# Optimization experiments

Measured on AMD Instinct MI355X. Metric: run time of the kernel, lower is better.

Reference implementation:

```python
import jax, jax.numpy as jnp
import numpy as np

K = 2            # top-k experts
TEMPERATURE = 1.0
EPS = 1e-9


def setup_inputs() -> dict:
    key = jax.random.key(0)
    k1, k2 = jax.random.split(key)
    B, S, D = 4, 4096, 4096
    G, E = 4, 64
    x = jax.random.normal(k1, (B, S, D), dtype=jnp.float32)
    # stacked gate weights, one [E, D] Linear weight per gate head
    W = jax.random.normal(k2, (G, E, D), dtype=jnp.float32) * 0.02
    return {"x": x, "W": W}


def reference(x, W):
    # per-head logits over experts: [B, S, G, E]; jitter disabled (eval / jitter_noise=0)
    logits = jnp.einsum('bsd,ged->bsge', x, W) * (1.0 / TEMPERATURE)
    probs = jax.nn.softmax(logits, axis=-1)          # softmax per head
    probs_full = probs.mean(axis=2)                  # consensus over heads: [B, S, E]
    topk_vals, idx = jax.lax.top_k(probs_full, K)    # sorted descending, matches aten.topk
    den = jnp.sum(topk_vals, axis=-1, keepdims=True)
    scores = topk_vals / jnp.maximum(den, EPS)       # clamp_min(den, 1e-9)
    pf = jax.lax.stop_gradient(probs_full)           # aux stats under no_grad
    importance = pf.mean(axis=(0, 1))                # [E]
    load = (pf > 0.0).astype(pf.dtype).mean(axis=(0, 1))  # [E]
    return idx, scores, probs_full, importance, load
```

## Files before the change

kernel.cpp:

```cpp
#include <hip/hip_runtime.h>

typedef _Float16 f16x8 __attribute__((ext_vector_type(8)));
typedef float    f32x4 __attribute__((ext_vector_type(4)));

#define MROWS 16384
#define NCOLS 256
#define KDIM  4096
#define BM    64
#define BK    32

#define OUT_SCORES 32768
#define OUT_PF     65536
#define OUT_IMP    1114112
#define OUT_LOAD   1114176

__global__ __launch_bounds__(256) void wprep(const float* __restrict__ W,
                                             _Float16* __restrict__ wfHi,
                                             _Float16* __restrict__ wfLo) {
    int t   = blockIdx.x * 256 + threadIdx.x;
    int l   = t & 63;
    int NT  = (t >> 6) & 15;
    int ksg = t >> 10;
    int n   = NT * 16 + (l & 15);
    int k   = ksg * 32 + ((l >> 4) << 3);
    const float* src = W + ((size_t)n * KDIM + (size_t)k);
    f16x8 hi, lo;
#pragma unroll
    for (int j = 0; j < 8; ++j) {
        float x = src[j];
        _Float16 h = (_Float16)x;
        hi[j] = h;
        lo[j] = (_Float16)(x - (float)h);
    }
    *(f16x8*)(wfHi + (size_t)t * 8) = hi;
    *(f16x8*)(wfLo + (size_t)t * 8) = lo;
}

__global__ __launch_bounds__(256, 4) void gemm3(const float* __restrict__ X,
        const _Float16* __restrict__ wfHi, const _Float16* __restrict__ wfLo,
        float* __restrict__ lsplit, int kQ) {
    __shared__ _Float16 aHi[2][2048];
    __shared__ _Float16 aLo[2][2048];

    const int tid  = threadIdx.x;
    const int lane = tid & 63;
    const int w    = tid >> 6;
    const int mt   = blockIdx.x & 255;
    const int s    = blockIdx.x >> 8;
    const int m0   = mt * BM;
    const int k0   = s * kQ;
    const int iters = kQ / BK;

    f32x4 acc[4][4];
#pragma unroll
    for (int a = 0; a < 4; ++a)
#pragma unroll
        for (int b = 0; b < 4; ++b) acc[a][b] = (f32x4){0.f, 0.f, 0.f, 0.f};

    const int sr = tid >> 2;
    const int c  = tid & 3;
    const float* xrow = X + ((size_t)(m0 + sr) * KDIM + (size_t)k0 + c * 8);
    const int wgran = (((sr >> 4) * 4 + c) * 16 + (sr & 15)) * 8;

    size_t bbase = ((size_t)(k0 >> 5) * 1024 + (size_t)w * 256 + (size_t)lane) * 8;
    const _Float16* pBH = wfHi + bbase;
    const _Float16* pBL = wfLo + bbase;

    {
        f32x4 v0 = *(const f32x4*)(xrow);
        f32x4 v1 = *(const f32x4*)(xrow + 4);
        f16x8 h, l;
#pragma unroll
        for (int j = 0; j < 4; ++j) {
            _Float16 ha = (_Float16)v0[j];
            h[j] = ha; l[j] = (_Float16)(v0[j] - (float)ha);
            _Float16 hb = (_Float16)v1[j];
            h[4 + j] = hb; l[4 + j] = (_Float16)(v1[j] - (float)hb);
        }
        *(f16x8*)(&aHi[0][wgran]) = h;
        *(f16x8*)(&aLo[0][wgran]) = l;
    }
    __syncthreads();

    for (int i = 0; i < iters; ++i) {
        const int cur = i & 1;

        f16x8 bH[4], bL[4];
#pragma unroll
        for (int ni = 0; ni < 4; ++ni) {
            bH[ni] = *(const f16x8*)(pBH + (size_t)ni * 512);
            bL[ni] = *(const f16x8*)(pBL + (size_t)ni * 512);
        }
        pBH += 8192;
        pBL += 8192;

        f32x4 nx0, nx1;
        const bool more = (i + 1 < iters);
        if (more) {
            const float* xp = xrow + (size_t)(i + 1) * BK;
            nx0 = *(const f32x4*)(xp);
            nx1 = *(const f32x4*)(xp + 4);
        }

#pragma unroll
        for (int mi = 0; mi < 4; ++mi) {
            f16x8 aH = *(const f16x8*)(&aHi[cur][(mi * 64 + lane) * 8]);
            f16x8 aL = *(const f16x8*)(&aLo[cur][(mi * 64 + lane) * 8]);
#pragma unroll
            for (int ni = 0; ni < 4; ++ni) {
                acc[mi][ni] = __builtin_amdgcn_mfma_f32_16x16x32_f16(aH, bH[ni], acc[mi][ni], 0, 0, 0);
                acc[mi][ni] = __builtin_amdgcn_mfma_f32_16x16x32_f16(aH, bL[ni], acc[mi][ni], 0, 0, 0);
                acc[mi][ni] = __builtin_amdgcn_mfma_f32_16x16x32_f16(aL, bH[ni], acc[mi][ni], 0, 0, 0);
            }
        }

        if (more) {
            const int nxt = cur ^ 1;
            f16x8 h, l;
#pragma unroll
            for (int j = 0; j < 4; ++j) {
                _Float16 ha = (_Float16)nx0[j];
                h[j] = ha; l[j] = (_Float16)(nx0[j] - (float)ha);
                _Float16 hb = (_Float16)nx1[j];
                h[4 + j] = hb; l[4 + j] = (_Float16)(nx1[j] - (float)hb);
            }
            *(f16x8*)(&aHi[nxt][wgran]) = h;
            *(f16x8*)(&aLo[nxt][wgran]) = l;
        }
        __syncthreads();
    }

    float* outp = lsplit + (size_t)s * ((size_t)MROWS * NCOLS);
#pragma unroll
    for (int mi = 0; mi < 4; ++mi) {
#pragma unroll
        for (int ni = 0; ni < 4; ++ni) {
            int col   = w * 64 + ni * 16 + (lane & 15);
            int rbase = m0 + mi * 16 + ((lane >> 4) << 2);
#pragma unroll
            for (int r = 0; r < 4; ++r)
                outp[(size_t)(rbase + r) * NCOLS + col] = acc[mi][ni][r];
        }
    }
}

__global__ __launch_bounds__(256) void finalize(const float* __restrict__ lsplit,
                                                int nsplit, float* __restrict__ out) {
    __shared__ float sImp[64], sLoad[64];
    const int tid  = threadIdx.x;
    const int lane = tid & 63;
    const int wv   = tid >> 6;
    if (tid < 64) { sImp[tid] = 0.f; sLoad[tid] = 0.f; }
    __syncthreads();

    const size_t SZ = (size_t)MROWS * NCOLS;
    const int r0 = blockIdx.x * 64 + wv * 16;

    f32x4 impAcc = (f32x4){0.f, 0.f, 0.f, 0.f};
    f32x4 ldAcc  = (f32x4){0.f, 0.f, 0.f, 0.f};

    for (int rr = 0; rr < 16; ++rr) {
        const int r = r0 + rr;
        const float* base = lsplit + (size_t)r * NCOLS + lane * 4;
        f32x4 a = *(const f32x4*)(base);
        for (int s = 1; s < nsplit; ++s)
            a += *(const f32x4*)(base + (size_t)s * SZ);

        float m = fmaxf(fmaxf(a[0], a[1]), fmaxf(a[2], a[3]));
#pragma unroll
        for (int msk = 1; msk < 16; msk <<= 1)
            m = fmaxf(m, __shfl_xor(m, msk));
        f32x4 p;
        float sa = 0.f;
#pragma unroll
        for (int j = 0; j < 4; ++j) { p[j] = __expf(a[j] - m); sa += p[j]; }
#pragma unroll
        for (int msk = 1; msk < 16; msk <<= 1)
            sa += __shfl_xor(sa, msk);
        float inv = 1.f / sa;
#pragma unroll
        for (int j = 0; j < 4; ++j) p[j] *= inv;

        f32x4 pf;
#pragma unroll
        for (int j = 0; j < 4; ++j) {
            float t = p[j];
            t += __shfl_xor(t, 16);
            t += __shfl_xor(t, 32);
            pf[j] = t * 0.25f;
        }

        if (lane < 16)
            *(f32x4*)(out + OUT_PF + (size_t)r * 64 + lane * 4) = pf;
        impAcc += pf;
#pragma unroll
        for (int j = 0; j < 4; ++j) ldAcc[j] += (pf[j] > 0.f) ? 1.f : 0.f;

        float v1 = -3.4e38f, v2 = -3.4e38f; int e1 = 0, e2 = 0;
#pragma unroll
        for (int j = 0; j < 4; ++j) {
            int e = 4 * (lane & 15) + j; float val = pf[j];
            if (val > v1) { v2 = v1; e2 = e1; v1 = val; e1 = e; }
            else if (val > v2) { v2 = val; e2 = e; }
        }
#pragma unroll
        for (int msk = 1; msk < 16; msk <<= 1) {
            float o1 = __shfl_xor(v1, msk); int oe1 = __shfl_xor(e1, msk);
            float o2 = __shfl_xor(v2, msk); int oe2 = __shfl_xor(e2, msk);
            bool ob = (o1 > v1) || (o1 == v1 && oe1 < e1);
            if (ob) {
                bool vb = (v1 > o2) || (v1 == o2 && e1 < oe2);
                v2 = vb ? v1 : o2; e2 = vb ? e1 : oe2;
                v1 = o1; e1 = oe1;
            } else {
                bool nb = (o1 > v2) || (o1 == v2 && oe1 < e2);
                v2 = nb ? o1 : v2; e2 = nb ? oe1 : e2;
            }
        }
        if (lane == 0) {
            float den = fmaxf(v1 + v2, 1e-9f);
            out[(size_t)r * 2]                  = (float)e1;
            out[(size_t)r * 2 + 1]              = (float)e2;
            out[OUT_SCORES + (size_t)r * 2]     = v1 / den;
            out[OUT_SCORES + (size_t)r * 2 + 1] = v2 / den;
        }
    }

    if (lane < 16) {
#pragma unroll
        for (int j = 0; j < 4; ++j) {
            atomicAdd(&sImp[4 * lane + j],  impAcc[j]);
            atomicAdd(&sLoad[4 * lane + j], ldAcc[j]);
        }
    }
    __syncthreads();
    if (tid < 64) {
        atomicAdd(out + OUT_IMP  + tid, sImp[tid]  * (1.0f / 16384.0f));
        atomicAdd(out + OUT_LOAD + tid, sLoad[tid] * (1.0f / 16384.0f));
    }
}

extern "C" void kernel_launch(void* const* d_in, const int* in_sizes, int n_in,
                              void* d_out, int out_size, void* d_ws, size_t ws_size,
                              hipStream_t stream) {
    const float* X = (const float*)d_in[0];
    const float* W = (const float*)d_in[1];
    float* out = (float*)d_out;
    char* ws = (char*)d_ws;

    _Float16* wfHi = (_Float16*)ws;
    _Float16* wfLo = (_Float16*)(ws + (2u << 20));
    float* lsplit  = (float*)(ws + (4u << 20));

    const size_t per = 16u << 20;
    int nsplit = (ws_size >= (4u << 20) + 4 * per) ? 4
               : (ws_size >= (4u << 20) + 2 * per) ? 2 : 1;

    hipMemsetAsync((void*)(out + OUT_IMP), 0, 128 * sizeof(float), stream);

    wprep<<<512, 256, 0, stream>>>(W, wfHi, wfLo);
    gemm3<<<256 * nsplit, 256, 0, stream>>>(X, wfHi, wfLo, lsplit, KDIM / nsplit);
    finalize<<<256, 256, 0, stream>>>(lsplit, nsplit, out);
}
```

Measured before the change: 460.5 us.

## Fuse softmax/top-k epilogue into GEMM, drop split-K, halve M tile

```diff
diff --git a/kernel.cpp b/kernel.cpp
--- a/kernel.cpp
+++ b/kernel.cpp
@@ -1,13 +1,16 @@
 #include <hip/hip_runtime.h>
 
 typedef _Float16 f16x8 __attribute__((ext_vector_type(8)));
+typedef _Float16 f16x4 __attribute__((ext_vector_type(4)));
 typedef float    f32x4 __attribute__((ext_vector_type(4)));
 
 #define MROWS 16384
 #define NCOLS 256
 #define KDIM  4096
-#define BM    64
+#define BM    32
 #define BK    32
+#define ITERS (KDIM / BK)
+#define LDP   264
 
 #define OUT_SCORES 32768
 #define OUT_PF     65536
@@ -36,202 +39,193 @@
     *(f16x8*)(wfLo + (size_t)t * 8) = lo;
 }
 
-__global__ __launch_bounds__(256, 4) void gemm3(const float* __restrict__ X,
+__device__ inline void cvt4(const f32x4 v, f16x4& hi, f16x4& lo) {
+#pragma unroll
+    for (int j = 0; j < 4; ++j) {
+        _Float16 h = (_Float16)v[j];
+        hi[j] = h;
+        lo[j] = (_Float16)(v[j] - (float)h);
+    }
+}
+
+__global__ __launch_bounds__(256, 2) void gemm_fused(const float* __restrict__ X,
         const _Float16* __restrict__ wfHi, const _Float16* __restrict__ wfLo,
-        float* __restrict__ lsplit, int kQ) {
-    __shared__ _Float16 aHi[2][2048];
-    __shared__ _Float16 aLo[2][2048];
+        float* __restrict__ out) {
+    __shared__ _Float16 aHi[2][BM * BK];
+    __shared__ _Float16 aLo[2][BM * BK];
+    __shared__ float P[BM * LDP];
+    __shared__ float sImp[64], sLoad[64];
 
     const int tid  = threadIdx.x;
     const int lane = tid & 63;
     const int w    = tid >> 6;
-    const int mt   = blockIdx.x & 255;
-    const int s    = blockIdx.x >> 8;
-    const int m0   = mt * BM;
-    const int k0   = s * kQ;
-    const int iters = kQ / BK;
-
-    f32x4 acc[4][4];
-#pragma unroll
-    for (int a = 0; a < 4; ++a)
+    const int m0   = blockIdx.x * BM;
+
+    f32x4 acc[2][4];
+#pragma unroll
+    for (int a = 0; a < 2; ++a)
 #pragma unroll
         for (int b = 0; b < 4; ++b) acc[a][b] = (f32x4){0.f, 0.f, 0.f, 0.f};
 
-    const int sr = tid >> 2;
-    const int c  = tid & 3;
-    const float* xrow = X + ((size_t)(m0 + sr) * KDIM + (size_t)k0 + c * 8);
-    const int wgran = (((sr >> 4) * 4 + c) * 16 + (sr & 15)) * 8;
-
-    size_t bbase = ((size_t)(k0 >> 5) * 1024 + (size_t)w * 256 + (size_t)lane) * 8;
-    const _Float16* pBH = wfHi + bbase;
-    const _Float16* pBL = wfLo + bbase;
+    const int g    = tid >> 1;
+    const int h    = tid & 1;
+    const int srow = ((g >> 6) << 4) + (g & 15);
+    const int kst  = ((g >> 4) & 3) * 8 + h * 4;
+    const float* xptr = X + ((size_t)(m0 + srow) * KDIM + kst);
+    const int wo = g * 8 + h * 4;
+
+    const _Float16* pBH = wfHi + ((size_t)w * 256 + (size_t)lane) * 8;
+    const _Float16* pBL = wfLo + ((size_t)w * 256 + (size_t)lane) * 8;
 
     {
-        f32x4 v0 = *(const f32x4*)(xrow);
-        f32x4 v1 = *(const f32x4*)(xrow + 4);
-        f16x8 h, l;
-#pragma unroll
-        for (int j = 0; j < 4; ++j) {
-            _Float16 ha = (_Float16)v0[j];
-            h[j] = ha; l[j] = (_Float16)(v0[j] - (float)ha);
-            _Float16 hb = (_Float16)v1[j];
-            h[4 + j] = hb; l[4 + j] = (_Float16)(v1[j] - (float)hb);
-        }
-        *(f16x8*)(&aHi[0][wgran]) = h;
-        *(f16x8*)(&aLo[0][wgran]) = l;
+        f32x4 v = *(const f32x4*)xptr;
+        f16x4 hi, lo; cvt4(v, hi, lo);
+        *(f16x4*)(&aHi[0][wo]) = hi;
+        *(f16x4*)(&aLo[0][wo]) = lo;
+    }
+    f32x4 nxs0, nxs1;
+    nxs1 = *(const f32x4*)(xptr + BK);
+    nxs0 = nxs1;
+    f16x8 bHc[4], bLc[4];
+#pragma unroll
+    for (int ni = 0; ni < 4; ++ni) {
+        bHc[ni] = *(const f16x8*)(pBH + ni * 512);
+        bLc[ni] = *(const f16x8*)(pBL + ni * 512);
     }
     __syncthreads();
 
-    for (int i = 0; i < iters; ++i) {
-        const int cur = i & 1;
-
-        f16x8 bH[4], bL[4];
+#pragma unroll 2
+    for (int i = 0; i < ITERS; ++i) {
+        const int cur = i & 1, nxt = cur ^ 1;
+
+        const int ipf = (i + 2 < ITERS) ? i + 2 : ITERS - 1;
+        f32x4 xin = *(const f32x4*)(xptr + (size_t)ipf * BK);
+
+        const int ibn = (i + 1 < ITERS) ? i + 1 : i;
+        const _Float16* nBH = pBH + (size_t)ibn * 8192;
+        const _Float16* nBL = pBL + (size_t)ibn * 8192;
+        f16x8 bHn[4], bLn[4];
 #pragma unroll
         for (int ni = 0; ni < 4; ++ni) {
-            bH[ni] = *(const f16x8*)(pBH + (size_t)ni * 512);
-            bL[ni] = *(const f16x8*)(pBL + (size_t)ni * 512);
-        }
-        pBH += 8192;
-        pBL += 8192;
-
-        f32x4 nx0, nx1;
-        const bool more = (i + 1 < iters);
-        if (more) {
-            const float* xp = xrow + (size_t)(i + 1) * BK;
-            nx0 = *(const f32x4*)(xp);
-            nx1 = *(const f32x4*)(xp + 4);
-        }
-
-#pragma unroll
-        for (int mi = 0; mi < 4; ++mi) {
+            bHn[ni] = *(const f16x8*)(nBH + ni * 512);
+            bLn[ni] = *(const f16x8*)(nBL + ni * 512);
+        }
+
+#pragma unroll
+        for (int mi = 0; mi < 2; ++mi) {
             f16x8 aH = *(const f16x8*)(&aHi[cur][(mi * 64 + lane) * 8]);
             f16x8 aL = *(const f16x8*)(&aLo[cur][(mi * 64 + lane) * 8]);
 #pragma unroll
             for (int ni = 0; ni < 4; ++ni) {
-                acc[mi][ni] = __builtin_amdgcn_mfma_f32_16x16x32_f16(aH, bH[ni], acc[mi][ni], 0, 0, 0);
-                acc[mi][ni] = __builtin_amdgcn_mfma_f32_16x16x32_f16(aH, bL[ni], acc[mi][ni], 0, 0, 0);
-                acc[mi][ni] = __builtin_amdgcn_mfma_f32_16x16x32_f16(aL, bH[ni], acc[mi][ni], 0, 0, 0);
+                acc[mi][ni] = __builtin_amdgcn_mfma_f32_16x16x32_f16(aH, bHc[ni], acc[mi][ni], 0, 0, 0);
+                acc[mi][ni] = __builtin_amdgcn_mfma_f32_16x16x32_f16(aH, bLc[ni], acc[mi][ni], 0, 0, 0);
+                acc[mi][ni] = __builtin_amdgcn_mfma_f32_16x16x32_f16(aL, bHc[ni], acc[mi][ni], 0, 0, 0);
             }
         }
 
-        if (more) {
-            const int nxt = cur ^ 1;
-            f16x8 h, l;
-#pragma unroll
-            for (int j = 0; j < 4; ++j) {
-                _Float16 ha = (_Float16)nx0[j];
-                h[j] = ha; l[j] = (_Float16)(nx0[j] - (float)ha);
-                _Float16 hb = (_Float16)nx1[j];
-                h[4 + j] = hb; l[4 + j] = (_Float16)(nx1[j] - (float)hb);
-            }
-            *(f16x8*)(&aHi[nxt][wgran]) = h;
-            *(f16x8*)(&aLo[nxt][wgran]) = l;
-        }
+        if (i + 1 < ITERS) {
+            f32x4 xv = ((i & 1) == 0) ? nxs1 : nxs0;
+            f16x4 hi, lo; cvt4(xv, hi, lo);
+            *(f16x4*)(&aHi[nxt][wo]) = hi;
+            *(f16x4*)(&aLo[nxt][wo]) = lo;
+        }
+        if ((i & 1) == 0) nxs0 = xin; else nxs1 = xin;
+#pragma unroll
+        for (int ni = 0; ni < 4; ++ni) { bHc[ni] = bHn[ni]; bLc[ni] = bLn[ni]; }
         __syncthreads();
     }
 
-    float* outp = lsplit + (size_t)s * ((size_t)MROWS * NCOLS);
-#pragma unroll
-    for (int mi = 0; mi < 4; ++mi) {
-#pragma unroll
-        for (int ni = 0; ni < 4; ++ni) {
-            int col   = w * 64 + ni * 16 + (lane & 15);
-            int rbase = m0 + mi * 16 + ((lane >> 4) << 2);
-#pragma unroll
-            for (int r = 0; r < 4; ++r)
-                outp[(size_t)(rbase + r) * NCOLS + col] = acc[mi][ni][r];
-        }
-    }
-}
-
-__global__ __launch_bounds__(256) void finalize(const float* __restrict__ lsplit,
-                                                int nsplit, float* __restrict__ out) {
-    __shared__ float sImp[64], sLoad[64];
-    const int tid  = threadIdx.x;
-    const int lane = tid & 63;
-    const int wv   = tid >> 6;
     if (tid < 64) { sImp[tid] = 0.f; sLoad[tid] = 0.f; }
+
+    const int qr = (lane >> 4) << 2;
+#pragma unroll
+    for (int mi = 0; mi < 2; ++mi) {
+#pragma unroll
+        for (int r = 0; r < 4; ++r) {
+            float m = fmaxf(fmaxf(acc[mi][0][r], acc[mi][1][r]),
+                            fmaxf(acc[mi][2][r], acc[mi][3][r]));
+#pragma unroll
+            for (int msk = 1; msk < 16; msk <<= 1)
+                m = fmaxf(m, __shfl_xor(m, msk));
+            float e[4], sa = 0.f;
+#pragma unroll
+            for (int ni = 0; ni < 4; ++ni) { e[ni] = __expf(acc[mi][ni][r] - m); sa += e[ni]; }
+#pragma unroll
+            for (int msk = 1; msk < 16; msk <<= 1)
+                sa += __shfl_xor(sa, msk);
+            float inv = 1.f / sa;
+            int rl = mi * 16 + qr + r;
+#pragma unroll
+            for (int ni = 0; ni < 4; ++ni)
+                P[rl * LDP + w * 64 + ni * 16 + (lane & 15)] = e[ni] * inv;
+        }
+    }
     __syncthreads();
 
-    const size_t SZ = (size_t)MROWS * NCOLS;
-    const int r0 = blockIdx.x * 64 + wv * 16;
-
-    f32x4 impAcc = (f32x4){0.f, 0.f, 0.f, 0.f};
-    f32x4 ldAcc  = (f32x4){0.f, 0.f, 0.f, 0.f};
-
-    for (int rr = 0; rr < 16; ++rr) {
-        const int r = r0 + rr;
-        const float* base = lsplit + (size_t)r * NCOLS + lane * 4;
-        f32x4 a = *(const f32x4*)(base);
-        for (int s = 1; s < nsplit; ++s)
-            a += *(const f32x4*)(base + (size_t)s * SZ);
-
-        float m = fmaxf(fmaxf(a[0], a[1]), fmaxf(a[2], a[3]));
-#pragma unroll
-        for (int msk = 1; msk < 16; msk <<= 1)
-            m = fmaxf(m, __shfl_xor(m, msk));
-        f32x4 p;
-        float sa = 0.f;
-#pragma unroll
-        for (int j = 0; j < 4; ++j) { p[j] = __expf(a[j] - m); sa += p[j]; }
-#pragma unroll
-        for (int msk = 1; msk < 16; msk <<= 1)
-            sa += __shfl_xor(sa, msk);
-        float inv = 1.f / sa;
-#pragma unroll
-        for (int j = 0; j < 4; ++j) p[j] *= inv;
-
-        f32x4 pf;
-#pragma unroll
-        for (int j = 0; j < 4; ++j) {
-            float t = p[j];
-            t += __shfl_xor(t, 16);
-            t += __shfl_xor(t, 32);
-            pf[j] = t * 0.25f;
-        }
-
-        if (lane < 16)
-            *(f32x4*)(out + OUT_PF + (size_t)r * 64 + lane * 4) = pf;
-        impAcc += pf;
-#pragma unroll
-        for (int j = 0; j < 4; ++j) ldAcc[j] += (pf[j] > 0.f) ? 1.f : 0.f;
-
-        float v1 = -3.4e38f, v2 = -3.4e38f; int e1 = 0, e2 = 0;
-#pragma unroll
-        for (int j = 0; j < 4; ++j) {
-            int e = 4 * (lane & 15) + j; float val = pf[j];
-            if (val > v1) { v2 = v1; e2 = e1; v1 = val; e1 = e; }
-            else if (val > v2) { v2 = val; e2 = e; }
-        }
-#pragma unroll
-        for (int msk = 1; msk < 16; msk <<= 1) {
-            float o1 = __shfl_xor(v1, msk); int oe1 = __shfl_xor(e1, msk);
-            float o2 = __shfl_xor(v2, msk); int oe2 = __shfl_xor(e2, msk);
-            bool ob = (o1 > v1) || (o1 == v1 && oe1 < e1);
-            if (ob) {
-                bool vb = (v1 > o2) || (v1 == o2 && e1 < oe2);
-                v2 = vb ? v1 : o2; e2 = vb ? e1 : oe2;
-                v1 = o1; e1 = oe1;
-            } else {
-                bool nb = (o1 > v2) || (o1 == v2 && oe1 < e2);
-                v2 = nb ? o1 : v2; e2 = nb ? oe1 : e2;
-            }
-        }
-        if (lane == 0) {
-            float den = fmaxf(v1 + v2, 1e-9f);
-            out[(size_t)r * 2]                  = (float)e1;
-            out[(size_t)r * 2 + 1]              = (float)e2;
-            out[OUT_SCORES + (size_t)r * 2]     = v1 / den;
-            out[OUT_SCORES + (size_t)r * 2 + 1] = v2 / den;
-        }
-    }
-
-    if (lane < 16) {
-#pragma unroll
-        for (int j = 0; j < 4; ++j) {
-            atomicAdd(&sImp[4 * lane + j],  impAcc[j]);
-            atomicAdd(&sLoad[4 * lane + j], ldAcc[j]);
-        }
+    const int rl = (w << 3) + (lane >> 3);
+    const int eb = (lane & 7) << 3;
+    const float* Prow = P + rl * LDP;
+    f32x4 pfa = (f32x4){0.f,0.f,0.f,0.f}, pfb = (f32x4){0.f,0.f,0.f,0.f};
+#pragma unroll
+    for (int gg = 0; gg < 4; ++gg) {
+        pfa += *(const f32x4*)(Prow + gg * 64 + eb);
+        pfb += *(const f32x4*)(Prow + gg * 64 + eb + 4);
+    }
+    pfa *= 0.25f; pfb *= 0.25f;
+
+    const int rg = m0 + rl;
+    *(f32x4*)(out + OUT_PF + (size_t)rg * 64 + eb)     = pfa;
+    *(f32x4*)(out + OUT_PF + (size_t)rg * 64 + eb + 4) = pfb;
+
+    float ia[8], la[8];
+#pragma unroll
+    for (int j = 0; j < 4; ++j) {
+        ia[j]     = pfa[j]; la[j]     = (pfa[j] > 0.f) ? 1.f : 0.f;
+        ia[4 + j] = pfb[j]; la[4 + j] = (pfb[j] > 0.f) ? 1.f : 0.f;
+    }
+#pragma unroll
+    for (int msk = 8; msk < 64; msk <<= 1)
+#pragma unroll
+        for (int j = 0; j < 8; ++j) {
+            ia[j] += __shfl_xor(ia[j], msk);
+            la[j] += __shfl_xor(la[j], msk);
+        }
+    if ((lane >> 3) == 0) {
+#pragma unroll
+        for (int j = 0; j < 8; ++j) {
+            atomicAdd(&sImp[eb + j],  ia[j]);
+            atomicAdd(&sLoad[eb + j], la[j]);
+        }
+    }
+
+    float v1 = -3.4e38f, v2 = -3.4e38f; int e1 = 0, e2 = 0;
+#pragma unroll
+    for (int j = 0; j < 8; ++j) {
+        float val = (j < 4) ? pfa[j] : pfb[j - 4];
+        int e = eb + j;
+        if (val > v1) { v2 = v1; e2 = e1; v1 = val; e1 = e; }
+        else if (val > v2) { v2 = val; e2 = e; }
+    }
+#pragma unroll
+    for (int msk = 1; msk < 8; msk <<= 1) {
+        float o1 = __shfl_xor(v1, msk); int oe1 = __shfl_xor(e1, msk);
+        float o2 = __shfl_xor(v2, msk); int oe2 = __shfl_xor(e2, msk);
+        bool ob = (o1 > v1) || (o1 == v1 && oe1 < e1);
+        if (ob) {
+            bool vb = (v1 > o2) || (v1 == o2 && e1 < oe2);
+            v2 = vb ? v1 : o2; e2 = vb ? e1 : oe2;
+            v1 = o1; e1 = oe1;
+        } else {
+            bool nb = (o1 > v2) || (o1 == v2 && oe1 < e2);
+            v2 = nb ? o1 : v2; e2 = nb ? oe1 : e2;
+        }
+    }
+    if ((lane & 7) == 0) {
+        float den = fmaxf(v1 + v2, 1e-9f);
+        out[(size_t)rg * 2]                  = (float)e1;
+        out[(size_t)rg * 2 + 1]              = (float)e2;
+        out[OUT_SCORES + (size_t)rg * 2]     = v1 / den;
+        out[OUT_SCORES + (size_t)rg * 2 + 1] = v2 / den;
     }
     __syncthreads();
     if (tid < 64) {
@@ -250,15 +244,9 @@
 
     _Float16* wfHi = (_Float16*)ws;
     _Float16* wfLo = (_Float16*)(ws + (2u << 20));
-    float* lsplit  = (float*)(ws + (4u << 20));
-
-    const size_t per = 16u << 20;
-    int nsplit = (ws_size >= (4u << 20) + 4 * per) ? 4
-               : (ws_size >= (4u << 20) + 2 * per) ? 2 : 1;
 
     hipMemsetAsync((void*)(out + OUT_IMP), 0, 128 * sizeof(float), stream);
 
     wprep<<<512, 256, 0, stream>>>(W, wfHi, wfLo);
-    gemm3<<<256 * nsplit, 256, 0, stream>>>(X, wfHi, wfLo, lsplit, KDIM / nsplit);
-    finalize<<<256, 256, 0, stream>>>(lsplit, nsplit, out);
-}
+    gemm_fused<<<512, 256, 0, stream>>>(X, wfHi, wfLo, out);
+}
```

Result: no change. 466.6 us (+1.3%).
